# Optimization experiments

Hardware: AMD Instinct MI355X
Metric: run time of the kernel (lower is better)

## Reference

```python
import jax, jax.numpy as jnp
import numpy as np

T_VALUES = (2.0, 8.0, 32.0, 128.0)
EPS = 1e-05
N_BANDS = 128


def setup_inputs() -> dict:
    key = jax.random.key(0)
    k1, k2, k3, k4 = jax.random.split(key, 4)
    x = jax.random.uniform(k1, (8, N_BANDS, 8192), dtype=jnp.float32)
    # Parameters are stored in log-space, matching the torch module's init
    # (log(alpha), log(delta), log(r) broadcast to n_bands).
    log_alpha = jnp.full((N_BANDS,), np.log(0.8), dtype=jnp.float32)
    log_delta = jnp.full((N_BANDS,), np.log(10.0), dtype=jnp.float32)
    log_r = jnp.full((N_BANDS,), np.log(0.25), dtype=jnp.float32)
    return {"x": x, "log_alpha": log_alpha, "log_delta": log_delta, "log_r": log_r}


def reference(x, log_alpha, log_delta, log_r):
    # x: [B, F, N]  (batch, bands, time frames)
    t_vals = jnp.asarray(T_VALUES, dtype=x.dtype)
    # s = (sqrt(1 + 4 t^2) - 1) / (2 t^2)  -- smoothing coefficient per rate
    s_vals = (jnp.sqrt(1.0 + 4.0 * t_vals ** 2) - 1.0) / (2.0 * t_vals ** 2)

    alpha = jnp.exp(log_alpha)[:, None]  # [F, 1]
    delta = jnp.exp(log_delta)[:, None]
    r = jnp.exp(log_r)[:, None]

    xt = jnp.moveaxis(x, -1, 0)  # [N, B, F], scan over time

    def ema(s):
        # IIR recursion m[t] = s*x[t] + (1-s)*m[t-1], m[-1] = x[0].
        # This is exactly what the torch triangular-matmul formulation computes:
        # smoother[t] = s * sum_{i<=t} x[i] (1-s)^{t-i} + (1-s)^{t+1} x[0].
        def step(m, xi):
            m = s * xi + (1.0 - s) * m
            return m, m
        _, ys = jax.lax.scan(step, xt[0], xt)
        return jnp.moveaxis(ys, 0, -1)  # [B, F, N]

    smoother = jax.vmap(ema)(s_vals)  # [T, B, F, N]

    # smooth = (eps + smoother)^(-alpha), written as in the source via log1p
    smooth = jnp.exp(-alpha * (jnp.log(EPS) + jnp.log1p(smoother / EPS)))
    pcen = (x[None] * smooth + delta) ** r - delta ** r  # [T, B, F, N]
    return jnp.transpose(pcen, (1, 0, 2, 3))  # [B, T, F, N]
```

## Files before the change

kernel.cpp:

```cpp
#include <hip/hip_runtime.h>

#define NB    128
#define NT    8192
#define TPB   256
#define CHUNK 32

__device__ __forceinline__ int swz(int n) { return n ^ (((n >> 5) & 7) << 2); }

__global__ __launch_bounds__(TPB, 4) void mrpcen_kernel(
    const float* __restrict__ x,
    const float* __restrict__ log_alpha,
    const float* __restrict__ log_delta,
    const float* __restrict__ log_r,
    float* __restrict__ out)
{
    __shared__ __align__(16) float sh[NT];
    __shared__ float sWagg[4];

    const int tid  = threadIdx.x;
    const int lane = tid & 63;
    const int wid  = tid >> 6;

    const int bft = blockIdx.x;
    const int t   = bft & 3;
    const int f   = (bft >> 2) & (NB - 1);
    const int b   = bft >> 9;

    const float* xrow = x + (size_t)(b * NB + f) * NT;

    const float alpha  = __expf(log_alpha[f]);
    const float r      = __expf(log_r[f]);
    const float delta  = __expf(log_delta[f]);
    const float deltar = __expf(r * log_delta[f]);

    const float tt = (float)(2 << (2 * t));
    const float t2 = tt * tt;
    const float s  = (sqrtf(1.f + 4.f * t2) - 1.f) / (2.f * t2);
    const float a1 = 1.f - s;
    float A = a1;
    A = A * A; A = A * A; A = A * A; A = A * A; A = A * A;

#pragma unroll
    for (int k = 0; k < 8; k++) {
        int n = k * 1024 + tid * 4;
        float4 v = *reinterpret_cast<const float4*>(xrow + n);
        *reinterpret_cast<float4*>(&sh[swz(n)]) = v;
    }
    __syncthreads();

    const float x0 = sh[0];

    float xc[CHUNK];
#pragma unroll
    for (int j = 0; j < 8; j++) {
        int n = tid * CHUNK + 4 * j;
        float4 v = *reinterpret_cast<const float4*>(&sh[swz(n)]);
        xc[4 * j + 0] = v.x; xc[4 * j + 1] = v.y;
        xc[4 * j + 2] = v.z; xc[4 * j + 3] = v.w;
    }

    float Bl = 0.f;
#pragma unroll
    for (int i = 0; i < CHUNK; i++)
        Bl = s * xc[i] + a1 * Bl;

    float v = Bl;
    float ap = A;
#pragma unroll
    for (int d = 1; d < 64; d <<= 1) {
        float up = __shfl_up(v, d);
        if (lane >= d) v += ap * up;
        ap *= ap;
    }
    const float a64 = ap;
    if (lane == 63) sWagg[wid] = v;
    __syncthreads();

    const float W0 = sWagg[0], W1 = sWagg[1], W2 = sWagg[2];
    float pre = 0.f;
    if (wid >= 1) pre = W0;
    if (wid >= 2) pre = a64 * pre + W1;
    if (wid >= 3) pre = a64 * pre + W2;

    float pl = 1.f, base = A;
    int e = lane;
#pragma unroll
    for (int bit = 0; bit < 6; bit++) {
        if (e & 1) pl *= base;
        base *= base;
        e >>= 1;
    }
    float aw = 1.f;
    const float a128 = a64 * a64;
    if (wid & 1) aw *= a64;
    if (wid & 2) aw *= a128;

    const float vprev = __shfl_up(v, 1);
    float m = pl * (aw * x0 + pre) + ((lane > 0) ? vprev : 0.f);

#pragma unroll
    for (int j = 0; j < 8; j++) {
        float ov[4];
#pragma unroll
        for (int q = 0; q < 4; q++) {
            float xi = xc[4 * j + q];
            m = s * xi + a1 * m;
            float smooth = __expf(-alpha * __logf(1e-5f + m));
            ov[q] = __expf(r * __logf(xi * smooth + delta)) - deltar;
        }
        *reinterpret_cast<float4*>(&sh[swz(tid * CHUNK + 4 * j)]) =
            make_float4(ov[0], ov[1], ov[2], ov[3]);
    }
    __syncthreads();

    float* oplane = out + (((size_t)b * 4 + t) * NB + f) * (size_t)NT;
#pragma unroll
    for (int k = 0; k < 8; k++) {
        int n = k * 1024 + tid * 4;
        float4 o = *reinterpret_cast<const float4*>(&sh[swz(n)]);
        *reinterpret_cast<float4*>(oplane + n) = o;
    }
}

extern "C" void kernel_launch(void* const* d_in, const int* in_sizes, int n_in,
                              void* d_out, int out_size, void* d_ws, size_t ws_size,
                              hipStream_t stream) {
    const float* x         = (const float*)d_in[0];
    const float* log_alpha = (const float*)d_in[1];
    const float* log_delta = (const float*)d_in[2];
    const float* log_r     = (const float*)d_in[3];
    float* out = (float*)d_out;

    mrpcen_kernel<<<dim3(8 * NB * 4), dim3(TPB), 0, stream>>>(
        x, log_alpha, log_delta, log_r, out);
}
```

Measured before the change: 169.0 us.

## Use 512-thread blocks with 16-element chunks, direct loads, and hardware exp2/log2

Doubles threads per block and halves the per-thread chunk, so each row is scanned with eight waves instead of four. Each thread now loads its chunk straight from global memory instead of staging the row through shared memory first. The cross-wave prefix combine and the per-wave decay factors are generalised to eight waves. The transcendental math now calls the AMD exp2/log2 builtins directly. The final barrier is dropped by having each wave write out only the shared-memory region it filled. The intent is to cut the serial scan length and barrier count and to raise occupancy. The cost is less coalesced global loads (each thread reads 64 contiguous bytes) and a longer cross-wave combine.

```diff
diff --git a/kernel.cpp b/kernel.cpp
--- a/kernel.cpp
+++ b/kernel.cpp
@@ -2,12 +2,15 @@
 
 #define NB    128
 #define NT    8192
-#define TPB   256
-#define CHUNK 32
+#define TPB   512
+#define CHUNK 16
+
+__device__ __forceinline__ float fexp2(float x) { return __builtin_amdgcn_exp2f(x); }
+__device__ __forceinline__ float flog2(float x) { return __builtin_amdgcn_logf(x); }
 
 __device__ __forceinline__ int swz(int n) { return n ^ (((n >> 5) & 7) << 2); }
 
-__global__ __launch_bounds__(TPB, 4) void mrpcen_kernel(
+__global__ __launch_bounds__(TPB, 8) void mrpcen_kernel(
     const float* __restrict__ x,
     const float* __restrict__ log_alpha,
     const float* __restrict__ log_delta,
@@ -15,7 +18,7 @@
     float* __restrict__ out)
 {
     __shared__ __align__(16) float sh[NT];
-    __shared__ float sWagg[4];
+    __shared__ float sWagg[8];
 
     const int tid  = threadIdx.x;
     const int lane = tid & 63;
@@ -32,32 +35,23 @@
     const float r      = __expf(log_r[f]);
     const float delta  = __expf(log_delta[f]);
     const float deltar = __expf(r * log_delta[f]);
+    const float nalpha = -alpha;
 
     const float tt = (float)(2 << (2 * t));
     const float t2 = tt * tt;
     const float s  = (sqrtf(1.f + 4.f * t2) - 1.f) / (2.f * t2);
     const float a1 = 1.f - s;
     float A = a1;
-    A = A * A; A = A * A; A = A * A; A = A * A; A = A * A;
-
-#pragma unroll
-    for (int k = 0; k < 8; k++) {
-        int n = k * 1024 + tid * 4;
-        float4 v = *reinterpret_cast<const float4*>(xrow + n);
-        *reinterpret_cast<float4*>(&sh[swz(n)]) = v;
-    }
-    __syncthreads();
-
-    const float x0 = sh[0];
+    A = A * A; A = A * A; A = A * A; A = A * A;
 
     float xc[CHUNK];
 #pragma unroll
-    for (int j = 0; j < 8; j++) {
-        int n = tid * CHUNK + 4 * j;
-        float4 v = *reinterpret_cast<const float4*>(&sh[swz(n)]);
+    for (int j = 0; j < 4; j++) {
+        float4 v = *reinterpret_cast<const float4*>(xrow + tid * CHUNK + 4 * j);
         xc[4 * j + 0] = v.x; xc[4 * j + 1] = v.y;
         xc[4 * j + 2] = v.z; xc[4 * j + 3] = v.w;
     }
+    const float x0 = xrow[0];
 
     float Bl = 0.f;
 #pragma unroll
@@ -76,11 +70,10 @@
     if (lane == 63) sWagg[wid] = v;
     __syncthreads();
 
-    const float W0 = sWagg[0], W1 = sWagg[1], W2 = sWagg[2];
     float pre = 0.f;
-    if (wid >= 1) pre = W0;
-    if (wid >= 2) pre = a64 * pre + W1;
-    if (wid >= 3) pre = a64 * pre + W2;
+#pragma unroll
+    for (int k = 0; k < 7; k++)
+        if (wid > k) pre = a64 * pre + sWagg[k];
 
     float pl = 1.f, base = A;
     int e = lane;
@@ -90,33 +83,37 @@
         base *= base;
         e >>= 1;
     }
-    float aw = 1.f;
-    const float a128 = a64 * a64;
-    if (wid & 1) aw *= a64;
-    if (wid & 2) aw *= a128;
+    float aw = 1.f, wb = a64;
+    e = wid;
+#pragma unroll
+    for (int bit = 0; bit < 3; bit++) {
+        if (e & 1) aw *= wb;
+        wb *= wb;
+        e >>= 1;
+    }
 
     const float vprev = __shfl_up(v, 1);
     float m = pl * (aw * x0 + pre) + ((lane > 0) ? vprev : 0.f);
 
 #pragma unroll
-    for (int j = 0; j < 8; j++) {
+    for (int j = 0; j < 4; j++) {
         float ov[4];
 #pragma unroll
         for (int q = 0; q < 4; q++) {
             float xi = xc[4 * j + q];
             m = s * xi + a1 * m;
-            float smooth = __expf(-alpha * __logf(1e-5f + m));
-            ov[q] = __expf(r * __logf(xi * smooth + delta)) - deltar;
+            float smooth = fexp2(nalpha * flog2(1e-5f + m));
+            ov[q] = fexp2(r * flog2(xi * smooth + delta)) - deltar;
         }
         *reinterpret_cast<float4*>(&sh[swz(tid * CHUNK + 4 * j)]) =
             make_float4(ov[0], ov[1], ov[2], ov[3]);
     }
-    __syncthreads();
 
     float* oplane = out + (((size_t)b * 4 + t) * NB + f) * (size_t)NT;
+    const int wbase = wid << 10;
 #pragma unroll
-    for (int k = 0; k < 8; k++) {
-        int n = k * 1024 + tid * 4;
+    for (int k = 0; k < 4; k++) {
+        int n = wbase + k * 256 + lane * 4;
         float4 o = *reinterpret_cast<const float4*>(&sh[swz(n)]);
         *reinterpret_cast<float4*>(oplane + n) = o;
     }
```

After: 163.8 us. 1.03x faster.
